# Performance work log

Hardware: AMD Instinct MI355X
Metric: run time of the kernel (lower is better)

The kernel has to match this reference:

```python
import jax, jax.numpy as jnp
import numpy as np

ALPHA = 0.2  # LeakyReLU negative slope

def setup_inputs() -> dict:
    key = jax.random.key(0)
    k_h, k_adj, k_W, k_a = jax.random.split(key, 4)
    B, N, F_in, F_out = 8, 2048, 256, 64
    h = jax.random.normal(k_h, (B, N, F_in), dtype=jnp.float32)
    adj = jax.random.randint(k_adj, (B, N, N), 0, 2, dtype=jnp.int32)
    # nn.Linear weights: W [F_out, F_in], a [1, 2*F_out]
    W = jax.random.normal(k_W, (F_out, F_in), dtype=jnp.float32) * (1.0 / np.sqrt(F_in))
    a = jax.random.normal(k_a, (1, 2 * F_out), dtype=jnp.float32) * (1.0 / np.sqrt(2 * F_out))
    return {"h": h, "adj": adj, "W": W, "a": a}

def reference(h, adj, W, a):
    # Wh = h @ W^T : [B, N, F_out]
    Wh = jnp.einsum('bnf,of->bno', h, W)
    F_out = Wh.shape[-1]
    # a([Wi, Wj]) decomposes: e_ij = a_i . Wh_i + a_j . Wh_j (no O(N^2 * 2F) concat)
    a_i = a[0, :F_out]   # [F_out]
    a_j = a[0, F_out:]   # [F_out]
    e_i = Wh @ a_i       # [B, N]
    e_j = Wh @ a_j       # [B, N]
    e = jax.nn.leaky_relu(e_i[:, :, None] + e_j[:, None, :], negative_slope=ALPHA)  # [B, N, N]
    e = jnp.where(adj == 0, -jnp.inf, e)
    att = jnp.nan_to_num(jax.nn.softmax(e, axis=-1), nan=0.0)
    # dropout is identity in eval mode
    return jnp.einsum('bnm,bmo->bno', att, Wh)
```

## Files before the change

### kernel.cpp

```cpp
#include <hip/hip_runtime.h>

typedef float f32x4 __attribute__((ext_vector_type(4)));
typedef __bf16 bf16x8 __attribute__((ext_vector_type(8)));
typedef int i32x4 __attribute__((ext_vector_type(4)));
typedef unsigned short u16;
typedef unsigned int u32;

#define ALPHA 0.2f

__device__ __forceinline__ u16 f2bf(float x) {
    u32 u = __float_as_uint(x);
    u += 0x7FFFu + ((u >> 16) & 1u);
    return (u16)(u >> 16);
}

__global__ __launch_bounds__(256) void k_wh(
    const float* __restrict__ hsrc, const float* __restrict__ Wsrc,
    const float* __restrict__ asrc,
    u16* __restrict__ WhbT,
    float* __restrict__ ei, float* __restrict__ ej)
{
    __shared__ float Wl[64][68];
    __shared__ float hl[64][68];
    __shared__ __align__(16) u16 tl[4096];

    const int tid = threadIdx.x;
    const int tx = tid & 15, ty = tid >> 4;
    const int R0 = blockIdx.x * 64;

    float acc[4][4] = {};

    for (int kc = 0; kc < 4; ++kc) {
        const int k0 = kc * 64;
        __syncthreads();
        #pragma unroll
        for (int p = 0; p < 4; ++p) {
            int idx = p * 1024 + tid * 4;
            int row = idx >> 6, k = idx & 63;
            float4 wv4 = *reinterpret_cast<const float4*>(&Wsrc[row * 256 + k0 + k]);
            Wl[k + 0][row] = wv4.x; Wl[k + 1][row] = wv4.y;
            Wl[k + 2][row] = wv4.z; Wl[k + 3][row] = wv4.w;
            float4 hv4 = *reinterpret_cast<const float4*>(&hsrc[(size_t)(R0 + row) * 256 + k0 + k]);
            hl[k + 0][row] = hv4.x; hl[k + 1][row] = hv4.y;
            hl[k + 2][row] = hv4.z; hl[k + 3][row] = hv4.w;
        }
        __syncthreads();
        #pragma unroll 4
        for (int k = 0; k < 64; ++k) {
            float4 hv = *reinterpret_cast<const float4*>(&hl[k][4 * ty]);
            float4 wv = *reinterpret_cast<const float4*>(&Wl[k][4 * tx]);
            float hr[4] = {hv.x, hv.y, hv.z, hv.w};
            float wc[4] = {wv.x, wv.y, wv.z, wv.w};
            #pragma unroll
            for (int i = 0; i < 4; ++i)
                #pragma unroll
                for (int j = 0; j < 4; ++j)
                    acc[i][j] = fmaf(hr[i], wc[j], acc[i][j]);
        }
    }

    float4 av_i = *reinterpret_cast<const float4*>(&asrc[4 * tx]);
    float4 av_j = *reinterpret_cast<const float4*>(&asrc[64 + 4 * tx]);
    #pragma unroll
    for (int i = 0; i < 4; ++i) {
        float pi = acc[i][0]*av_i.x + acc[i][1]*av_i.y + acc[i][2]*av_i.z + acc[i][3]*av_i.w;
        float pj = acc[i][0]*av_j.x + acc[i][1]*av_j.y + acc[i][2]*av_j.z + acc[i][3]*av_j.w;
        #pragma unroll
        for (int off = 1; off < 16; off <<= 1) {
            pi += __shfl_xor(pi, off, 64);
            pj += __shfl_xor(pj, off, 64);
        }
        if (tx == 0) {
            ei[R0 + 4 * ty + i] = pi;
            ej[R0 + 4 * ty + i] = pj;
        }
    }

    #pragma unroll
    for (int i = 0; i < 4; ++i)
        #pragma unroll
        for (int j = 0; j < 4; ++j) {
            int row = 4 * tx + j;
            int col = 4 * ty + i;
            tl[(row * 64 + col) ^ ((row & 7) << 3)] = f2bf(acc[i][j]);
        }
    __syncthreads();
    {
        const int b = blockIdx.x >> 5;
        const int nloc = (blockIdx.x & 31) * 64;
        const int o = tid >> 2, rg = tid & 3;
        #pragma unroll
        for (int c = 0; c < 2; ++c) {
            int u = (o * 64 + rg * 16 + 8 * c) ^ ((o & 7) << 3);
            int4 v = *reinterpret_cast<const int4*>(&tl[u]);
            *reinterpret_cast<int4*>(&WhbT[(size_t)(b * 64 + o) * 2048 + nloc + rg * 16 + 8 * c]) = v;
        }
    }
}

__global__ __launch_bounds__(256) void k_attn(
    const int* __restrict__ adj, const u16* __restrict__ WhbT,
    const float* __restrict__ ei_g, const float* __restrict__ ej_g,
    float* __restrict__ nump, float* __restrict__ denp)
{
    __shared__ __align__(16) u16 whl[64 * 264];
    __shared__ __align__(16) float ejl[1024];

    const int tid  = threadIdx.x;
    const int lane = tid & 63;
    const int w    = tid >> 6;
    const int lb = (blockIdx.x & 7) * 64 + (blockIdx.x >> 3);
    const int mt = lb & 1;
    const int nt = (lb >> 1) & 31;
    const int b  = lb >> 6;
    const int r  = lane & 15;
    const int ks = lane >> 4;
    const int m0 = mt * 1024;

    {
        float4 v = *reinterpret_cast<const float4*>(&ej_g[b * 2048 + m0 + tid * 4]);
        *reinterpret_cast<float4*>(&ejl[tid * 4]) = v;
    }

    const u16* whb = WhbT + (size_t)b * 131072;
    const int sf = tid >> 2;
    const int su = (tid & 3) * 8;
    int4 pv0, pv1, pv2, pv3, pv4, pv5, pv6, pv7;
#define PLOAD(p) { const u16* pp = whb + sf * 2048 + m0 + (p) * 256 + su * 8; \
    pv0 = *reinterpret_cast<const int4*>(pp);      pv1 = *reinterpret_cast<const int4*>(pp + 8); \
    pv2 = *reinterpret_cast<const int4*>(pp + 16); pv3 = *reinterpret_cast<const int4*>(pp + 24); \
    pv4 = *reinterpret_cast<const int4*>(pp + 32); pv5 = *reinterpret_cast<const int4*>(pp + 40); \
    pv6 = *reinterpret_cast<const int4*>(pp + 48); pv7 = *reinterpret_cast<const int4*>(pp + 56); }
#define PWRITE() { char* wp = reinterpret_cast<char*>(whl) + sf * 528 + su * 16; \
    *reinterpret_cast<int4*>(wp)       = pv0; *reinterpret_cast<int4*>(wp + 16)  = pv1; \
    *reinterpret_cast<int4*>(wp + 32)  = pv2; *reinterpret_cast<int4*>(wp + 48)  = pv3; \
    *reinterpret_cast<int4*>(wp + 64)  = pv4; *reinterpret_cast<int4*>(wp + 80)  = pv5; \
    *reinterpret_cast<int4*>(wp + 96)  = pv6; *reinterpret_cast<int4*>(wp + 112) = pv7; }
    PLOAD(0);

    float mj = -1e30f;
    #pragma unroll
    for (int i = 0; i < 8; ++i) {
        float4 v = *reinterpret_cast<const float4*>(&ej_g[b * 2048 + (i * 64 + lane) * 4]);
        mj = fmaxf(mj, fmaxf(fmaxf(v.x, v.y), fmaxf(v.z, v.w)));
    }
    #pragma unroll
    for (int off = 1; off < 64; off <<= 1) mj = fmaxf(mj, __shfl_xor(mj, off, 64));

    const float eiv = ei_g[b * 2048 + nt * 64 + w * 16 + r];
    const float xM  = eiv + mj;
    const float M   = fmaxf(xM, ALPHA * xM);

    bf16x8 bones;
    {
        const float o = (r == 0) ? 1.0f : 0.0f;
        #pragma unroll
        for (int j = 0; j < 8; ++j) bones[j] = (__bf16)o;
    }

    const int* adjp = adj + (size_t)(b * 2048 + nt * 64 + w * 16 + r) * 2048 + m0 + ks * 8;

    i32x4 Aa0, Aa1, Ba0, Ba1, Ca0, Ca1, Da0, Da1;
#define LADJ(gt, x0, x1) if ((gt) < 32) { \
    x0 = __builtin_nontemporal_load(reinterpret_cast<const i32x4*>(adjp + (gt) * 32)); \
    x1 = __builtin_nontemporal_load(reinterpret_cast<const i32x4*>(adjp + (gt) * 32 + 4)); }
    LADJ(0, Aa0, Aa1); LADJ(1, Ba0, Ba1); LADJ(2, Ca0, Ca1); LADJ(3, Da0, Da1);

    PWRITE();
    __syncthreads();

    f32x4 acc0 = {}, acc1 = {}, acc2 = {}, acc3 = {}, acc4 = {};

    const char* wl0 = reinterpret_cast<const char*>(whl) + r * 528 + ks * 16;
    const float* eb = ejl + ks * 8;

#define PVAL(mk, ev, dst) { \
    float e_ = eiv + (ev); \
    float lr_ = fmaxf(e_, ALPHA * e_); \
    float p_ = __expf(lr_ - M); \
    dst = (__bf16)(((mk) != 0) ? p_ : 0.0f); }

#define STEP(gt, x0, x1) { \
    const int tl_ = (gt) & 7; \
    float4 e0 = *reinterpret_cast<const float4*>(eb + (gt) * 32); \
    float4 e1 = *reinterpret_cast<const float4*>(eb + (gt) * 32 + 4); \
    bf16x8 af; \
    PVAL(x0[0], e0.x, af[0]); PVAL(x0[1], e0.y, af[1]); \
    PVAL(x0[2], e0.z, af[2]); PVAL(x0[3], e0.w, af[3]); \
    PVAL(x1[0], e1.x, af[4]); PVAL(x1[1], e1.y, af[5]); \
    PVAL(x1[2], e1.z, af[6]); PVAL(x1[3], e1.w, af[7]); \
    bf16x8 w0 = *reinterpret_cast<const bf16x8*>(wl0 + tl_ * 64); \
    bf16x8 w1 = *reinterpret_cast<const bf16x8*>(wl0 + tl_ * 64 + 16 * 528); \
    bf16x8 w2 = *reinterpret_cast<const bf16x8*>(wl0 + tl_ * 64 + 32 * 528); \
    bf16x8 w3 = *reinterpret_cast<const bf16x8*>(wl0 + tl_ * 64 + 48 * 528); \
    acc0 = __builtin_amdgcn_mfma_f32_16x16x32_bf16(af, w0, acc0, 0, 0, 0); \
    acc1 = __builtin_amdgcn_mfma_f32_16x16x32_bf16(af, w1, acc1, 0, 0, 0); \
    acc2 = __builtin_amdgcn_mfma_f32_16x16x32_bf16(af, w2, acc2, 0, 0, 0); \
    acc3 = __builtin_amdgcn_mfma_f32_16x16x32_bf16(af, w3, acc3, 0, 0, 0); \
    acc4 = __builtin_amdgcn_mfma_f32_16x16x32_bf16(af, bones, acc4, 0, 0, 0); }

    #pragma unroll
    for (int p = 0; p < 4; ++p) {
        if (p < 3) PLOAD(p + 1);
        STEP(p * 8 + 0, Aa0, Aa1); LADJ(p * 8 + 4,  Aa0, Aa1);
        STEP(p * 8 + 1, Ba0, Ba1); LADJ(p * 8 + 5,  Ba0, Ba1);
        STEP(p * 8 + 2, Ca0, Ca1); LADJ(p * 8 + 6,  Ca0, Ca1);
        STEP(p * 8 + 3, Da0, Da1); LADJ(p * 8 + 7,  Da0, Da1);
        STEP(p * 8 + 4, Aa0, Aa1); LADJ(p * 8 + 8,  Aa0, Aa1);
        STEP(p * 8 + 5, Ba0, Ba1); LADJ(p * 8 + 9,  Ba0, Ba1);
        STEP(p * 8 + 6, Ca0, Ca1); LADJ(p * 8 + 10, Ca0, Ca1);
        STEP(p * 8 + 7, Da0, Da1); LADJ(p * 8 + 11, Da0, Da1);
        if (p < 3) {
            __syncthreads();
            PWRITE();
            __syncthreads();
        }
    }
#undef STEP
#undef PVAL
#undef LADJ
#undef PWRITE
#undef PLOAD

    const size_t nb0 = (size_t)mt * 16384 + b * 2048 + nt * 64 + w * 16;
    #pragma unroll
    for (int q = 0; q < 4; ++q) {
        const int rr = ks * 4 + q;
        float* np = nump + (nb0 + rr) * 64 + r;
        np[0]  = acc0[q];
        np[16] = acc1[q];
        np[32] = acc2[q];
        np[48] = acc3[q];
        if (r == 0) denp[nb0 + rr] = acc4[q];
    }
}

__global__ __launch_bounds__(256) void k_norm(
    const float* __restrict__ nump, const float* __restrict__ denp,
    float* __restrict__ out)
{
    const int tid = threadIdx.x;
    const int f4 = tid & 15;
    const size_t N = (size_t)blockIdx.x * 16 + (tid >> 4);
    const float d = denp[N] + denp[16384 + N];
    const float inv = (d > 0.0f) ? 1.0f / d : 0.0f;
    float4 a = *reinterpret_cast<const float4*>(&nump[N * 64 + f4 * 4]);
    float4 c = *reinterpret_cast<const float4*>(&nump[(16384 + N) * 64 + f4 * 4]);
    float4 o;
    o.x = (a.x + c.x) * inv; o.y = (a.y + c.y) * inv;
    o.z = (a.z + c.z) * inv; o.w = (a.w + c.w) * inv;
    *reinterpret_cast<float4*>(&out[N * 64 + f4 * 4]) = o;
}

extern "C" void kernel_launch(void* const* d_in, const int* in_sizes, int n_in,
                              void* d_out, int out_size, void* d_ws, size_t ws_size,
                              hipStream_t stream)
{
    const float* h   = (const float*)d_in[0];
    const int*   adj = (const int*)d_in[1];
    const float* W   = (const float*)d_in[2];
    const float* a   = (const float*)d_in[3];
    float* out = (float*)d_out;

    u16*   WhbT = (u16*)d_ws;
    float* ei   = (float*)((char*)d_ws + 2 * 1024 * 1024);
    float* ej   = ei + 16384;
    float* nump = (float*)((char*)d_ws + 4 * 1024 * 1024);
    float* denp = (float*)((char*)d_ws + 12 * 1024 * 1024);

    k_wh  <<<dim3(256),  dim3(256), 0, stream>>>(h, W, a, WhbT, ei, ej);
    k_attn<<<dim3(512),  dim3(256), 0, stream>>>(adj, WhbT, ei, ej, nump, denp);
    k_norm<<<dim3(1024), dim3(256), 0, stream>>>(nump, denp, out);
}
```

Baseline: 64.91 us.

## Double-buffer Wh panels in LDS, deepen adj prefetch, use exp2

Splits the shared Wh panel buffer into two halves so the next panel is written into the idle buffer while the current one is consumed. Each panel switch then needs one barrier instead of two. The adjacency prefetch depth doubles from 4 to 8 tiles in flight. ej and ei are pre-scaled by log2(e) so the exponential can use exp2f. The cost is doubled LDS use and more registers, which may lower occupancy.

```diff
diff --git a/kernel.cpp b/kernel.cpp
--- a/kernel.cpp
+++ b/kernel.cpp
@@ -7,6 +7,7 @@
 typedef unsigned int u32;
 
 #define ALPHA 0.2f
+#define LOG2E 1.4426950408889634f
 
 __device__ __forceinline__ u16 f2bf(float x) {
     u32 u = __float_as_uint(x);
@@ -103,7 +104,7 @@
     const float* __restrict__ ei_g, const float* __restrict__ ej_g,
     float* __restrict__ nump, float* __restrict__ denp)
 {
-    __shared__ __align__(16) u16 whl[64 * 264];
+    __shared__ __align__(16) u16 whl[2 * 64 * 264];
     __shared__ __align__(16) float ejl[1024];
 
     const int tid  = threadIdx.x;
@@ -119,6 +120,7 @@
 
     {
         float4 v = *reinterpret_cast<const float4*>(&ej_g[b * 2048 + m0 + tid * 4]);
+        v.x *= LOG2E; v.y *= LOG2E; v.z *= LOG2E; v.w *= LOG2E;
         *reinterpret_cast<float4*>(&ejl[tid * 4]) = v;
     }
 
@@ -131,56 +133,64 @@
     pv2 = *reinterpret_cast<const int4*>(pp + 16); pv3 = *reinterpret_cast<const int4*>(pp + 24); \
     pv4 = *reinterpret_cast<const int4*>(pp + 32); pv5 = *reinterpret_cast<const int4*>(pp + 40); \
     pv6 = *reinterpret_cast<const int4*>(pp + 48); pv7 = *reinterpret_cast<const int4*>(pp + 56); }
-#define PWRITE() { char* wp = reinterpret_cast<char*>(whl) + sf * 528 + su * 16; \
+#define PWRITE(d) { char* wp = reinterpret_cast<char*>(whl) + (d) * 33792 + sf * 528 + su * 16; \
     *reinterpret_cast<int4*>(wp)       = pv0; *reinterpret_cast<int4*>(wp + 16)  = pv1; \
     *reinterpret_cast<int4*>(wp + 32)  = pv2; *reinterpret_cast<int4*>(wp + 48)  = pv3; \
     *reinterpret_cast<int4*>(wp + 64)  = pv4; *reinterpret_cast<int4*>(wp + 80)  = pv5; \
     *reinterpret_cast<int4*>(wp + 96)  = pv6; *reinterpret_cast<int4*>(wp + 112) = pv7; }
     PLOAD(0);
 
-    float mj = -1e30f;
-    #pragma unroll
-    for (int i = 0; i < 8; ++i) {
-        float4 v = *reinterpret_cast<const float4*>(&ej_g[b * 2048 + (i * 64 + lane) * 4]);
-        mj = fmaxf(mj, fmaxf(fmaxf(v.x, v.y), fmaxf(v.z, v.w)));
-    }
-    #pragma unroll
-    for (int off = 1; off < 64; off <<= 1) mj = fmaxf(mj, __shfl_xor(mj, off, 64));
-
-    const float eiv = ei_g[b * 2048 + nt * 64 + w * 16 + r];
-    const float xM  = eiv + mj;
-    const float M   = fmaxf(xM, ALPHA * xM);
-
-    bf16x8 bones;
-    {
-        const float o = (r == 0) ? 1.0f : 0.0f;
-        #pragma unroll
-        for (int j = 0; j < 8; ++j) bones[j] = (__bf16)o;
-    }
-
     const int* adjp = adj + (size_t)(b * 2048 + nt * 64 + w * 16 + r) * 2048 + m0 + ks * 8;
 
     i32x4 Aa0, Aa1, Ba0, Ba1, Ca0, Ca1, Da0, Da1;
+    i32x4 Ea0, Ea1, Fa0, Fa1, Ga0, Ga1, Ha0, Ha1;
 #define LADJ(gt, x0, x1) if ((gt) < 32) { \
     x0 = __builtin_nontemporal_load(reinterpret_cast<const i32x4*>(adjp + (gt) * 32)); \
     x1 = __builtin_nontemporal_load(reinterpret_cast<const i32x4*>(adjp + (gt) * 32 + 4)); }
     LADJ(0, Aa0, Aa1); LADJ(1, Ba0, Ba1); LADJ(2, Ca0, Ca1); LADJ(3, Da0, Da1);
-
-    PWRITE();
+    LADJ(4, Ea0, Ea1); LADJ(5, Fa0, Fa1); LADJ(6, Ga0, Ga1); LADJ(7, Ha0, Ha1);
+
+    float mj = -1e30f;
+    #pragma unroll
+    for (int i = 0; i < 8; ++i) {
+        float4 v = *reinterpret_cast<const float4*>(&ej_g[b * 2048 + (i * 64 + lane) * 4]);
+        mj = fmaxf(mj, fmaxf(fmaxf(v.x, v.y), fmaxf(v.z, v.w)));
+    }
+    #pragma unroll
+    for (int off = 1; off < 64; off <<= 1) mj = fmaxf(mj, __shfl_xor(mj, off, 64));
+
+    const float eiv2 = ei_g[b * 2048 + nt * 64 + w * 16 + r] * LOG2E;
+    const float xM2  = eiv2 + mj * LOG2E;
+    const float M2   = fmaxf(xM2, ALPHA * xM2);
+
+    bf16x8 bones;
+    {
+        const float o = (r == 0) ? 1.0f : 0.0f;
+        #pragma unroll
+        for (int j = 0; j < 8; ++j) bones[j] = (__bf16)o;
+    }
+
+    PWRITE(0);
     __syncthreads();
 
     f32x4 acc0 = {}, acc1 = {}, acc2 = {}, acc3 = {}, acc4 = {};
 
     const char* wl0 = reinterpret_cast<const char*>(whl) + r * 528 + ks * 16;
+    const char* wl1 = wl0 + 33792;
     const float* eb = ejl + ks * 8;
 
+#define PBAR() { asm volatile("s_waitcnt lgkmcnt(0)" ::: "memory"); \
+    __builtin_amdgcn_sched_barrier(0); \
+    __builtin_amdgcn_s_barrier(); \
+    __builtin_amdgcn_sched_barrier(0); }
+
 #define PVAL(mk, ev, dst) { \
-    float e_ = eiv + (ev); \
-    float lr_ = fmaxf(e_, ALPHA * e_); \
-    float p_ = __expf(lr_ - M); \
+    float x_ = eiv2 + (ev); \
+    float lr_ = fmaxf(x_, ALPHA * x_); \
+    float p_ = exp2f(lr_ - M2); \
     dst = (__bf16)(((mk) != 0) ? p_ : 0.0f); }
 
-#define STEP(gt, x0, x1) { \
+#define STEP(gt, x0, x1, wl) { \
     const int tl_ = (gt) & 7; \
     float4 e0 = *reinterpret_cast<const float4*>(eb + (gt) * 32); \
     float4 e1 = *reinterpret_cast<const float4*>(eb + (gt) * 32 + 4); \
@@ -189,35 +199,44 @@
     PVAL(x0[2], e0.z, af[2]); PVAL(x0[3], e0.w, af[3]); \
     PVAL(x1[0], e1.x, af[4]); PVAL(x1[1], e1.y, af[5]); \
     PVAL(x1[2], e1.z, af[6]); PVAL(x1[3], e1.w, af[7]); \
-    bf16x8 w0 = *reinterpret_cast<const bf16x8*>(wl0 + tl_ * 64); \
-    bf16x8 w1 = *reinterpret_cast<const bf16x8*>(wl0 + tl_ * 64 + 16 * 528); \
-    bf16x8 w2 = *reinterpret_cast<const bf16x8*>(wl0 + tl_ * 64 + 32 * 528); \
-    bf16x8 w3 = *reinterpret_cast<const bf16x8*>(wl0 + tl_ * 64 + 48 * 528); \
+    bf16x8 w0 = *reinterpret_cast<const bf16x8*>(wl + tl_ * 64); \
+    bf16x8 w1 = *reinterpret_cast<const bf16x8*>(wl + tl_ * 64 + 16 * 528); \
+    bf16x8 w2 = *reinterpret_cast<const bf16x8*>(wl + tl_ * 64 + 32 * 528); \
+    bf16x8 w3 = *reinterpret_cast<const bf16x8*>(wl + tl_ * 64 + 48 * 528); \
     acc0 = __builtin_amdgcn_mfma_f32_16x16x32_bf16(af, w0, acc0, 0, 0, 0); \
     acc1 = __builtin_amdgcn_mfma_f32_16x16x32_bf16(af, w1, acc1, 0, 0, 0); \
     acc2 = __builtin_amdgcn_mfma_f32_16x16x32_bf16(af, w2, acc2, 0, 0, 0); \
     acc3 = __builtin_amdgcn_mfma_f32_16x16x32_bf16(af, w3, acc3, 0, 0, 0); \
     acc4 = __builtin_amdgcn_mfma_f32_16x16x32_bf16(af, bones, acc4, 0, 0, 0); }
 
-    #pragma unroll
-    for (int p = 0; p < 4; ++p) {
-        if (p < 3) PLOAD(p + 1);
-        STEP(p * 8 + 0, Aa0, Aa1); LADJ(p * 8 + 4,  Aa0, Aa1);
-        STEP(p * 8 + 1, Ba0, Ba1); LADJ(p * 8 + 5,  Ba0, Ba1);
-        STEP(p * 8 + 2, Ca0, Ca1); LADJ(p * 8 + 6,  Ca0, Ca1);
-        STEP(p * 8 + 3, Da0, Da1); LADJ(p * 8 + 7,  Da0, Da1);
-        STEP(p * 8 + 4, Aa0, Aa1); LADJ(p * 8 + 8,  Aa0, Aa1);
-        STEP(p * 8 + 5, Ba0, Ba1); LADJ(p * 8 + 9,  Ba0, Ba1);
-        STEP(p * 8 + 6, Ca0, Ca1); LADJ(p * 8 + 10, Ca0, Ca1);
-        STEP(p * 8 + 7, Da0, Da1); LADJ(p * 8 + 11, Da0, Da1);
-        if (p < 3) {
-            __syncthreads();
-            PWRITE();
-            __syncthreads();
-        }
-    }
+#define PANEL8(base, wl) \
+    STEP((base)+0, Aa0, Aa1, wl); LADJ((base)+8,  Aa0, Aa1); \
+    STEP((base)+1, Ba0, Ba1, wl); LADJ((base)+9,  Ba0, Ba1); \
+    STEP((base)+2, Ca0, Ca1, wl); LADJ((base)+10, Ca0, Ca1); \
+    STEP((base)+3, Da0, Da1, wl); LADJ((base)+11, Da0, Da1); \
+    STEP((base)+4, Ea0, Ea1, wl); LADJ((base)+12, Ea0, Ea1); \
+    STEP((base)+5, Fa0, Fa1, wl); LADJ((base)+13, Fa0, Fa1); \
+    STEP((base)+6, Ga0, Ga1, wl); LADJ((base)+14, Ga0, Ga1); \
+    STEP((base)+7, Ha0, Ha1, wl); LADJ((base)+15, Ha0, Ha1);
+
+    PLOAD(1);
+    PANEL8(0, wl0);
+    PWRITE(1); PBAR();
+
+    PLOAD(2);
+    PANEL8(8, wl1);
+    PWRITE(0); PBAR();
+
+    PLOAD(3);
+    PANEL8(16, wl0);
+    PWRITE(1); PBAR();
+
+    PANEL8(24, wl1);
+
+#undef PANEL8
 #undef STEP
 #undef PVAL
+#undef PBAR
 #undef LADJ
 #undef PWRITE
 #undef PLOAD
```

Result: no change. 66.11 us (+1.8%).
